# Kernel tuning notes

Measured on AMD Instinct MI355X. Metric: run time of the kernel, lower is better.

The kernel has to match this reference:

```python
import jax, jax.numpy as jnp
import numpy as np

D_MODEL = 1024
NEG_INF = -1e9


def setup_inputs() -> dict:
    key = jax.random.key(0)
    ks = jax.random.split(key, 9)
    B, S, D = 8, 2048, D_MODEL
    q = jax.random.normal(ks[0], (B, S, D), dtype=jnp.float32)
    k = jax.random.normal(ks[1], (B, S, D), dtype=jnp.float32)
    v = jax.random.normal(ks[2], (B, S, D), dtype=jnp.float32)
    mask = jax.random.randint(ks[3], (B, S), 0, 2, dtype=jnp.int32)
    scale = 1.0 / np.sqrt(D)
    Wq = jax.random.normal(ks[4], (D, D), dtype=jnp.float32) * scale
    bq = jnp.zeros((D,), dtype=jnp.float32)
    Wout = jax.random.normal(ks[5], (D, D), dtype=jnp.float32) * scale
    bout = jnp.zeros((D,), dtype=jnp.float32)
    return {"q": q, "k": k, "v": v, "mask": mask,
            "Wq": Wq, "bq": bq, "Wout": Wout, "bout": bout}


def reference(q, k, v, mask, Wq, bq, Wout, bout):
    # Faithful to original: the SAME q_linear projects q, k and v.
    qp = jnp.einsum('bsd,ed->bse', q, Wq) + bq
    kp = jnp.einsum('bsd,ed->bse', k, Wq) + bq
    vp = jnp.einsum('bsd,ed->bse', v, Wq) + bq
    d_k = q.shape[-1]
    # original divides K by sqrt(d_k) before the matmul (same math as scaling scores)
    scores = jnp.einsum('bqd,bkd->bqk', qp, kp) / jnp.sqrt(jnp.float32(d_k))  # [B,Sq,Sk]
    m = mask[:, None, :]  # [B,1,Sk]
    scores = jnp.where(m == 0, jnp.float32(-1e9), scores)
    weights = jax.nn.softmax(scores, axis=-1)
    out = jnp.einsum('bqk,bkd->bqd', weights, vp)
    out = jnp.einsum('bqd,ed->bqe', out, Wout) + bout
    return (out, weights)
```

## Files before the change

kernel.cpp:

```cpp
#include <hip/hip_runtime.h>
#include <hip/hip_bf16.h>

typedef __attribute__((ext_vector_type(8))) short short8;
typedef __attribute__((ext_vector_type(4))) float f32x4;

#define S_LEN 2048
#define DM 1024
#define NBATCH 8

__device__ __forceinline__ ushort f2b(float f) {
    union { float f; unsigned u; } a; a.f = f;
    unsigned u = a.u;
    u += 0x7fffu + ((u >> 16) & 1u);
    return (ushort)(u >> 16);
}

__device__ __forceinline__ unsigned pkbf(float a, float b) {
    float2 t; t.x = a; t.y = b;
    __hip_bfloat162 h = __float22bfloat162_rn(t);
    union { __hip_bfloat162 h; unsigned u; } c; c.h = h;
    return c.u;
}

#define GLDS(gp, lp) __builtin_amdgcn_global_load_lds( \
    (const __attribute__((address_space(1))) void*)(gp), \
    (__attribute__((address_space(3))) void*)(lp), 16, 0, 0)

template<int OMODE, bool HAS_BIAS>
__global__ __launch_bounds__(512, 2) void gemm256(
    const ushort* __restrict__ A, const ushort* __restrict__ B,
    void* __restrict__ Cv, const float* __restrict__ bias,
    int K, int lda, int ldb, int ldc,
    long long sA, long long sB, long long sC)
{
    __shared__ __align__(16) ushort lA[2][256 * 32];
    __shared__ __align__(16) ushort lB[2][256 * 32];

    const int t = threadIdx.x;
    const int wid = t >> 6, lane = t & 63;
    const int wm = wid >> 2, wn = wid & 3;
    const int z = blockIdx.z;

    const int gx = gridDim.x, gy = gridDim.y;
    const int nwg = gx * gy;
    const int lid = blockIdx.y * gx + blockIdx.x;
    const int qq = nwg >> 3, r8 = nwg & 7;
    const int xcd = lid & 7, off = lid >> 3;
    const int w = (xcd < r8 ? xcd * (qq + 1) : r8 * (qq + 1) + (xcd - r8) * qq) + off;
    const int bm = w / gy, bn = w % gy;

    const ushort* Ap = A + (size_t)z * sA + (size_t)(bm * 256) * lda;
    const ushort* Bp = B + (size_t)z * sB + (size_t)(bn * 256) * ldb;

    f32x4 acc[8][4] = {};

    const int srow = t >> 2;
    const int scol = ((t & 3) ^ ((t >> 2) & 3)) * 8;
    const int nK = K >> 5;

    const int r = lane & 15;
    const int cb = ((lane >> 4) * 16) ^ ((r & 3) << 4);

    int cur = 0;
    {
        const ushort* ga = Ap + (size_t)srow * lda + scol;
        GLDS(ga, (char*)lA[0] + wid * 1024);
        GLDS(ga + (size_t)128 * lda, (char*)lA[0] + 8192 + wid * 1024);
        const ushort* gb = Bp + (size_t)srow * ldb + scol;
        GLDS(gb, (char*)lB[0] + wid * 1024);
        GLDS(gb + (size_t)128 * ldb, (char*)lB[0] + 8192 + wid * 1024);
    }
    __syncthreads();

    for (int kt = 0; kt < nK; ++kt) {
        if (kt + 1 < nK) {
            const int k0 = (kt + 1) * 32;
            const ushort* ga = Ap + (size_t)srow * lda + k0 + scol;
            char* dA = (char*)lA[cur ^ 1];
            GLDS(ga, dA + wid * 1024);
            GLDS(ga + (size_t)128 * lda, dA + 8192 + wid * 1024);
            const ushort* gb = Bp + (size_t)srow * ldb + k0 + scol;
            char* dB = (char*)lB[cur ^ 1];
            GLDS(gb, dB + wid * 1024);
            GLDS(gb + (size_t)128 * ldb, dB + 8192 + wid * 1024);
        }
        const char* la = (const char*)lA[cur];
        const char* lb = (const char*)lB[cur];
        short8 af[8], bfr[4];
#pragma unroll
        for (int m = 0; m < 8; m++) {
            const int row = wm * 128 + m * 16 + r;
            af[m] = *(const short8*)(la + row * 64 + cb);
        }
#pragma unroll
        for (int n = 0; n < 4; n++) {
            const int row = wn * 64 + n * 16 + r;
            bfr[n] = *(const short8*)(lb + row * 64 + cb);
        }
#pragma unroll
        for (int m = 0; m < 8; m++)
#pragma unroll
            for (int n = 0; n < 4; n++)
                acc[m][n] = __builtin_amdgcn_mfma_f32_16x16x32_bf16(af[m], bfr[n], acc[m][n], 0, 0, 0);
        __syncthreads();
        cur ^= 1;
    }

    const int ro = (lane >> 4) * 4;
    const int colb = bn * 256 + wn * 64;
    const int rowb = bm * 256 + wm * 128;
    float bv[4];
    if constexpr (HAS_BIAS) {
#pragma unroll
        for (int n = 0; n < 4; n++) bv[n] = bias[colb + n * 16 + r];
    }

    if constexpr (OMODE == 0) {
        float* Cp = (float*)Cv + (size_t)z * sC;
#pragma unroll
        for (int m = 0; m < 8; m++)
#pragma unroll
            for (int n = 0; n < 4; n++) {
                const int col = colb + n * 16 + r;
#pragma unroll
                for (int j = 0; j < 4; j++) {
                    float vv = acc[m][n][j];
                    if constexpr (HAS_BIAS) vv += bv[n];
                    Cp[(size_t)(rowb + m * 16 + ro + j) * ldc + col] = vv;
                }
            }
    } else if constexpr (OMODE == 1) {
        ushort* Cp = (ushort*)Cv + (size_t)z * sC;
#pragma unroll
        for (int m = 0; m < 8; m++)
#pragma unroll
            for (int n = 0; n < 4; n++) {
                const int col = colb + n * 16 + r;
#pragma unroll
                for (int j = 0; j < 4; j++) {
                    float vv = acc[m][n][j];
                    if constexpr (HAS_BIAS) vv += bv[n];
                    Cp[(size_t)(rowb + m * 16 + ro + j) * ldc + col] = f2b(vv);
                }
            }
    } else {
        ushort* Cp = (ushort*)Cv + (size_t)z * sC;
#pragma unroll
        for (int m = 0; m < 8; m++)
#pragma unroll
            for (int n = 0; n < 4; n++) {
                const int col = colb + n * 16 + r;
                float v0 = acc[m][n][0], v1 = acc[m][n][1], v2 = acc[m][n][2], v3 = acc[m][n][3];
                if constexpr (HAS_BIAS) { v0 += bv[n]; v1 += bv[n]; v2 += bv[n]; v3 += bv[n]; }
                ushort4 u;
                u.x = f2b(v0); u.y = f2b(v1); u.z = f2b(v2); u.w = f2b(v3);
                *(ushort4*)&Cp[(size_t)col * ldc + rowb + m * 16 + ro] = u;
            }
    }
}

__global__ __launch_bounds__(256) void cast_f32_bf16_k(
    const float* __restrict__ in, ushort* __restrict__ outp, int n)
{
    int idx = (blockIdx.x * 256 + threadIdx.x) * 4;
    if (idx >= n) return;
    float4 f = *(const float4*)&in[idx];
    uint2 u; u.x = pkbf(f.x, f.y); u.y = pkbf(f.z, f.w);
    *(uint2*)&outp[idx] = u;
}

__global__ __launch_bounds__(256) void cast3_k(
    const float* __restrict__ q, const float* __restrict__ k,
    const float* __restrict__ v, ushort* __restrict__ outp, int n_each)
{
    const float* src = (blockIdx.y == 0) ? q : (blockIdx.y == 1) ? k : v;
    ushort* dst = outp + (size_t)blockIdx.y * n_each;
    const int stride = gridDim.x * 256 * 4;
    for (int idx = (blockIdx.x * 256 + threadIdx.x) * 4; idx < n_each; idx += stride) {
        float4 f = *(const float4*)&src[idx];
        uint2 u; u.x = pkbf(f.x, f.y); u.y = pkbf(f.z, f.w);
        *(uint2*)&dst[idx] = u;
    }
}

__global__ __launch_bounds__(256) void softmax_rows(
    float* __restrict__ w, const int* __restrict__ mask, ushort* __restrict__ wb)
{
    __shared__ float red[8];
    const int rid = blockIdx.x;
    const int b = rid >> 11;
    float* row = w + (size_t)rid * S_LEN;
    ushort* brow = wb + (size_t)rid * S_LEN;
    const int* mrow = mask + (size_t)b * S_LEN;
    const int t = threadIdx.x;
    const int wid = t >> 6, lane = t & 63;
    const float scale = 0.03125f;

    float x[8];
    float mx = -3.0e38f;
#pragma unroll
    for (int i = 0; i < 2; i++) {
        const int idx = (t + i * 256) * 4;
        float4 s4 = *(const float4*)&row[idx];
        int4 m4 = *(const int4*)&mrow[idx];
        float* xp = &x[i * 4];
        xp[0] = (m4.x == 0) ? -1.0e9f : s4.x * scale;
        xp[1] = (m4.y == 0) ? -1.0e9f : s4.y * scale;
        xp[2] = (m4.z == 0) ? -1.0e9f : s4.z * scale;
        xp[3] = (m4.w == 0) ? -1.0e9f : s4.w * scale;
        mx = fmaxf(mx, fmaxf(fmaxf(xp[0], xp[1]), fmaxf(xp[2], xp[3])));
    }
#pragma unroll
    for (int off = 32; off; off >>= 1) mx = fmaxf(mx, __shfl_xor(mx, off));
    if (lane == 0) red[wid] = mx;
    __syncthreads();
    mx = fmaxf(fmaxf(red[0], red[1]), fmaxf(red[2], red[3]));

    float sum = 0.0f;
#pragma unroll
    for (int i = 0; i < 8; i++) { x[i] = __expf(x[i] - mx); sum += x[i]; }
#pragma unroll
    for (int off = 32; off; off >>= 1) sum += __shfl_xor(sum, off);
    if (lane == 0) red[4 + wid] = sum;
    __syncthreads();
    sum = red[4] + red[5] + red[6] + red[7];
    const float inv = 1.0f / sum;

#pragma unroll
    for (int i = 0; i < 2; i++) {
        const int idx = (t + i * 256) * 4;
        float4 o;
        o.x = x[i * 4 + 0] * inv; o.y = x[i * 4 + 1] * inv;
        o.z = x[i * 4 + 2] * inv; o.w = x[i * 4 + 3] * inv;
        *(float4*)&row[idx] = o;
        uint2 ub;
        ub.x = pkbf(o.x, o.y);
        ub.y = pkbf(o.z, o.w);
        *(uint2*)&brow[idx] = ub;
    }
}

extern "C" void kernel_launch(void* const* d_in, const int* in_sizes, int n_in,
                              void* d_out, int out_size, void* d_ws, size_t ws_size,
                              hipStream_t stream)
{
    const float* q    = (const float*)d_in[0];
    const float* k    = (const float*)d_in[1];
    const float* v    = (const float*)d_in[2];
    const int*   mask = (const int*)d_in[3];
    const float* Wq   = (const float*)d_in[4];
    const float* bq   = (const float*)d_in[5];
    const float* Wout = (const float*)d_in[6];
    const float* bout = (const float*)d_in[7];

    float* out     = (float*)d_out;
    float* weights = out + (size_t)NBATCH * S_LEN * DM;

    const size_t NTOK = (size_t)NBATCH * S_LEN;

    ushort* qkvb = (ushort*)weights;
    ushort* qb = qkvb;
    ushort* kb = qb + NTOK * DM;
    ushort* vb = kb + NTOK * DM;
    ushort* wbf = (ushort*)d_out;

    ushort* qp    = (ushort*)d_ws;
    ushort* kp    = qp + NTOK * DM;
    ushort* vpT   = kp + NTOK * DM;
    ushort* attn  = qp;
    ushort* Wqb   = vpT + NTOK * DM;
    ushort* Woutb = Wqb + (size_t)DM * DM;

    dim3 blk(256, 1, 1);
    dim3 blk5(512, 1, 1);

    cast_f32_bf16_k<<<dim3(1024, 1, 1), blk, 0, stream>>>(Wq, Wqb, DM * DM);
    cast_f32_bf16_k<<<dim3(1024, 1, 1), blk, 0, stream>>>(Wout, Woutb, DM * DM);
    cast3_k<<<dim3(2048, 3, 1), blk, 0, stream>>>(q, k, v, qkvb, (int)(NTOK * DM));

    gemm256<1, true><<<dim3(64, 4, 1), blk5, 0, stream>>>(
        qb, Wqb, qp, bq, 1024, 1024, 1024, 1024, 0, 0, 0);
    gemm256<1, true><<<dim3(64, 4, 1), blk5, 0, stream>>>(
        kb, Wqb, kp, bq, 1024, 1024, 1024, 1024, 0, 0, 0);
    gemm256<2, true><<<dim3(8, 4, NBATCH), blk5, 0, stream>>>(
        vb, Wqb, vpT, bq, 1024, 1024, 1024, 2048,
        (long long)S_LEN * DM, 0, (long long)DM * S_LEN);

    gemm256<0, false><<<dim3(8, 8, NBATCH), blk5, 0, stream>>>(
        qp, kp, weights, nullptr, 1024, 1024, 1024, 2048,
        (long long)S_LEN * DM, (long long)S_LEN * DM, (long long)S_LEN * S_LEN);

    softmax_rows<<<dim3(NBATCH * S_LEN, 1, 1), blk, 0, stream>>>(weights, mask, wbf);

    gemm256<1, false><<<dim3(8, 4, NBATCH), blk5, 0, stream>>>(
        wbf, vpT, attn, nullptr, 2048, 2048, 2048, 1024,
        (long long)S_LEN * S_LEN, (long long)DM * S_LEN, (long long)S_LEN * DM);

    gemm256<0, true><<<dim3(64, 4, 1), blk5, 0, stream>>>(
        attn, Woutb, out, bout, 1024, 1024, 1024, 1024, 0, 0, 0);
}
```

Baseline: 529.2 us.

## Deepen GEMM K-tile to 64 with wider swizzle and sub-tiled MFMA issue

The bf16 GEMM kernel now stages 64-wide K tiles into LDS instead of 32, with an 8-way XOR swizzle, so there are half as many barriers and pipeline iterations. The inner loop is split into m/n sub-blocks that load fragments just before use, which lowers peak fragment register pressure, and the MFMA bursts are wrapped in s_setprio. LDS use doubles to 128KB per block, which may reduce occupancy below the launch_bounds target of 2 blocks per CU.

```diff
diff --git a/kernel.cpp b/kernel.cpp
--- a/kernel.cpp
+++ b/kernel.cpp
@@ -33,11 +33,12 @@
     int K, int lda, int ldb, int ldc,
     long long sA, long long sB, long long sC)
 {
-    __shared__ __align__(16) ushort lA[2][256 * 32];
-    __shared__ __align__(16) ushort lB[2][256 * 32];
+    __shared__ __align__(16) ushort lA[2][256 * 64];
+    __shared__ __align__(16) ushort lB[2][256 * 64];
 
     const int t = threadIdx.x;
-    const int wid = t >> 6, lane = t & 63;
+    const int lane = t & 63;
+    const int wid = t >> 6;
     const int wm = wid >> 2, wn = wid & 3;
     const int z = blockIdx.z;
 
@@ -54,54 +55,67 @@
 
     f32x4 acc[8][4] = {};
 
-    const int srow = t >> 2;
-    const int scol = ((t & 3) ^ ((t >> 2) & 3)) * 8;
-    const int nK = K >> 5;
+    const int srow = t >> 3;
+    const int scol = (((t & 7) ^ (srow & 7))) * 8;
+    const int nK = K >> 6;
 
     const int r = lane & 15;
-    const int cb = ((lane >> 4) * 16) ^ ((r & 3) << 4);
+    const int swz = (r & 7) << 4;
+
+    auto stage = [&](int kt, int buf) {
+        const int k0 = kt * 64;
+        const ushort* ga = Ap + (size_t)srow * lda + k0 + scol;
+        char* dA = (char*)lA[buf];
+#pragma unroll
+        for (int i = 0; i < 4; i++)
+            GLDS(ga + (size_t)(64 * i) * lda, dA + i * 8192 + t * 16);
+        const ushort* gb = Bp + (size_t)srow * ldb + k0 + scol;
+        char* dB = (char*)lB[buf];
+#pragma unroll
+        for (int i = 0; i < 4; i++)
+            GLDS(gb + (size_t)(64 * i) * ldb, dB + i * 8192 + t * 16);
+    };
+
+    stage(0, 0);
+    __syncthreads();
 
     int cur = 0;
-    {
-        const ushort* ga = Ap + (size_t)srow * lda + scol;
-        GLDS(ga, (char*)lA[0] + wid * 1024);
-        GLDS(ga + (size_t)128 * lda, (char*)lA[0] + 8192 + wid * 1024);
-        const ushort* gb = Bp + (size_t)srow * ldb + scol;
-        GLDS(gb, (char*)lB[0] + wid * 1024);
-        GLDS(gb + (size_t)128 * ldb, (char*)lB[0] + 8192 + wid * 1024);
-    }
-    __syncthreads();
-
     for (int kt = 0; kt < nK; ++kt) {
-        if (kt + 1 < nK) {
-            const int k0 = (kt + 1) * 32;
-            const ushort* ga = Ap + (size_t)srow * lda + k0 + scol;
-            char* dA = (char*)lA[cur ^ 1];
-            GLDS(ga, dA + wid * 1024);
-            GLDS(ga + (size_t)128 * lda, dA + 8192 + wid * 1024);
-            const ushort* gb = Bp + (size_t)srow * ldb + k0 + scol;
-            char* dB = (char*)lB[cur ^ 1];
-            GLDS(gb, dB + wid * 1024);
-            GLDS(gb + (size_t)128 * ldb, dB + 8192 + wid * 1024);
-        }
+        if (kt + 1 < nK) stage(kt + 1, cur ^ 1);
         const char* la = (const char*)lA[cur];
         const char* lb = (const char*)lB[cur];
-        short8 af[8], bfr[4];
-#pragma unroll
-        for (int m = 0; m < 8; m++) {
-            const int row = wm * 128 + m * 16 + r;
-            af[m] = *(const short8*)(la + row * 64 + cb);
+#pragma unroll
+        for (int mh = 0; mh < 2; mh++) {
+            short8 af[4][2];
+#pragma unroll
+            for (int m = 0; m < 4; m++) {
+                const int row = wm * 128 + mh * 64 + m * 16 + r;
+#pragma unroll
+                for (int ks = 0; ks < 2; ks++)
+                    af[m][ks] = *(const short8*)(la + row * 128 + ((ks * 64 + (lane >> 4) * 16) ^ swz));
+            }
+#pragma unroll
+            for (int nh = 0; nh < 2; nh++) {
+                short8 bf[2][2];
+#pragma unroll
+                for (int n = 0; n < 2; n++) {
+                    const int row = wn * 64 + nh * 32 + n * 16 + r;
+#pragma unroll
+                    for (int ks = 0; ks < 2; ks++)
+                        bf[n][ks] = *(const short8*)(lb + row * 128 + ((ks * 64 + (lane >> 4) * 16) ^ swz));
+                }
+                __builtin_amdgcn_s_setprio(1);
+#pragma unroll
+                for (int m = 0; m < 4; m++)
+#pragma unroll
+                    for (int n = 0; n < 2; n++)
+#pragma unroll
+                        for (int ks = 0; ks < 2; ks++)
+                            acc[mh * 4 + m][nh * 2 + n] = __builtin_amdgcn_mfma_f32_16x16x32_bf16(
+                                af[m][ks], bf[n][ks], acc[mh * 4 + m][nh * 2 + n], 0, 0, 0);
+                __builtin_amdgcn_s_setprio(0);
+            }
         }
-#pragma unroll
-        for (int n = 0; n < 4; n++) {
-            const int row = wn * 64 + n * 16 + r;
-            bfr[n] = *(const short8*)(lb + row * 64 + cb);
-        }
-#pragma unroll
-        for (int m = 0; m < 8; m++)
-#pragma unroll
-            for (int n = 0; n < 4; n++)
-                acc[m][n] = __builtin_amdgcn_mfma_f32_16x16x32_bf16(af[m], bfr[n], acc[m][n], 0, 0, 0);
         __syncthreads();
         cur ^= 1;
     }
```

Measured after the change: 472.2 us. 1.12x faster.
